# Optimization experiments

Measured on AMD Instinct MI355X. Metric: run time of the kernel, lower is better.

The kernel has to match this reference:

```python
import jax, jax.numpy as jnp
import numpy as np

N, D_IN, D_H, K, E = 100000, 128, 256, 16, 3200000


def setup_inputs() -> dict:
    key = jax.random.key(0)
    ks = jax.random.split(key, 6)
    x = jax.random.normal(ks[0], (N, D_IN), dtype=jnp.float32)
    edge_index = jax.random.randint(ks[1], (2, E), 0, N, dtype=jnp.int64)
    # Linear params (stored as [in, out] for x @ W + b)
    W1 = jax.random.normal(ks[2], (D_IN, D_H), dtype=jnp.float32) * 0.05
    b1 = jnp.zeros((D_H,), dtype=jnp.float32)
    W2 = jax.random.normal(ks[3], (D_H, K), dtype=jnp.float32) * 0.05
    b2 = jnp.zeros((K,), dtype=jnp.float32)
    return {"x": x, "edge_index": edge_index, "W1": W1, "b1": b1, "W2": W2, "b2": b2}


def reference(x, edge_index, W1, b1, W2, b2):
    # 2-layer MLP + row softmax -> soft cluster assignments C [N, K]
    h = jax.nn.relu(x @ W1 + b1)
    C = jax.nn.softmax(h @ W2 + b2, axis=1)
    # trace((C C^T)^T @ adj) == sum over edges (u,v) of C[u] . C[v]
    # (exact, incl. duplicate edges, since to_dense_adj scatter-adds 1 per edge)
    src, dst = edge_index[0], edge_index[1]
    edge_sum = jnp.sum(C[src] * C[dst])  # [E, K] gathered dot products, reduced
    num_edges = jnp.asarray(edge_index.shape[1], dtype=C.dtype)  # adj.sum()
    modularity_loss = -edge_sum / num_edges
    return (C, modularity_loss)
```

## Files before the change

### kernel.cpp

```cpp
#include <hip/hip_runtime.h>

#define N_NODES 100000
#define D_INF   128
#define D_HID   256
#define K_CL    16
#define N_EDGES 3200000
#define N_TILES (N_NODES / 16)

typedef __attribute__((ext_vector_type(8))) __bf16  bf16x8;
typedef __attribute__((ext_vector_type(8))) unsigned short u16x8;
typedef __attribute__((ext_vector_type(4))) float   f32x4;

__device__ __forceinline__ unsigned short f2bf(float f) {
    unsigned int u = __builtin_bit_cast(unsigned int, f);
    u += 0x7fffu + ((u >> 16) & 1u);
    return (unsigned short)(u >> 16);
}
__device__ __forceinline__ float bflo(unsigned int p) {
    return __builtin_bit_cast(float, p << 16);
}
__device__ __forceinline__ float bfhi(unsigned int p) {
    return __builtin_bit_cast(float, p & 0xffff0000u);
}

__global__ void prep_kernel(const float* __restrict__ W1,
                            const float* __restrict__ W2,
                            unsigned short* __restrict__ w1t,
                            unsigned short* __restrict__ w2t,
                            float* __restrict__ acc)
{
    const int i = blockIdx.x * 256 + threadIdx.x;
    if (i == 0) *acc = 0.f;
    if (i < D_INF * D_HID) {
        const int n = i >> 7, k = i & 127;
        w1t[i] = f2bf(W1[k * D_HID + n]);
    }
    if (i < D_HID * K_CL) {
        const int t = i >> 8, n = i & 255;
        w2t[i] = f2bf(W2[n * K_CL + t]);
    }
}

#define W1S 136
#define CHS 40

__global__ __launch_bounds__(256, 2) void mlp_kernel(
    const float* __restrict__ x, const unsigned short* __restrict__ W1T,
    const float* __restrict__ b1, const unsigned short* __restrict__ W2T,
    const float* __restrict__ b2, float* __restrict__ C,
    unsigned short* __restrict__ Cb)
{
    __shared__ unsigned short w1s[256 * W1S];
    __shared__ unsigned short chbuf[4][2][16 * CHS];
    __shared__ float b1s[D_HID];

    const int tid  = threadIdx.x;
    const int wv   = tid >> 6;
    const int lane = tid & 63;
    const int c    = lane & 15;
    const int q    = lane >> 4;

    #pragma unroll
    for (int it = 0; it < 16; ++it) {
        const int idx = it * 256 + tid;
        const int row = idx >> 4, ch = idx & 15;
        const uint4 v = ((const uint4*)W1T)[idx];
        *(uint4*)&w1s[row * W1S + ch * 8] = v;
    }
    if (tid < D_HID) b1s[tid] = b1[tid];

    bf16x8 w2f[8];
    #pragma unroll
    for (int kc2 = 0; kc2 < 8; ++kc2)
        w2f[kc2] = *(const bf16x8*)(W2T + (size_t)c * D_HID + kc2 * 32 + q * 8);
    const float b2v = b2[c];
    __syncthreads();

    unsigned short* const chA = &chbuf[wv][0][0];
    unsigned short* const chB = &chbuf[wv][1][0];

    const int wid     = blockIdx.x * 4 + wv;
    const int wstride = gridDim.x * 4;

    for (int tile = wid; tile < N_TILES; tile += wstride) {
        const int m0 = tile * 16;

        const float* xrow = x + (size_t)(m0 + c) * D_INF + q * 8;
        bf16x8 afr[4];
        #pragma unroll
        for (int kc = 0; kc < 4; ++kc) {
            const float4 xa = *(const float4*)(xrow + kc * 32);
            const float4 xb = *(const float4*)(xrow + kc * 32 + 4);
            u16x8 af;
            af[0] = f2bf(xa.x); af[1] = f2bf(xa.y); af[2] = f2bf(xa.z); af[3] = f2bf(xa.w);
            af[4] = f2bf(xb.x); af[5] = f2bf(xb.y); af[6] = f2bf(xb.z); af[7] = f2bf(xb.w);
            afr[kc] = __builtin_bit_cast(bf16x8, af);
        }

        f32x4 acc2 = (f32x4){0.f, 0.f, 0.f, 0.f};
        #pragma unroll
        for (int kc2 = 0; kc2 < 8; ++kc2) {
            unsigned short* const cb = (kc2 & 1) ? chB : chA;
            #pragma unroll
            for (int half = 0; half < 2; ++half) {
                const int nt = kc2 * 2 + half;
                f32x4 a1 = (f32x4){0.f, 0.f, 0.f, 0.f};
                #pragma unroll
                for (int kc = 0; kc < 4; ++kc) {
                    const bf16x8 bf =
                        *(const bf16x8*)&w1s[(nt * 16 + c) * W1S + kc * 32 + q * 8];
                    a1 = __builtin_amdgcn_mfma_f32_16x16x32_bf16(afr[kc], bf, a1, 0, 0, 0);
                }
                const float bv = b1s[nt * 16 + c];
                #pragma unroll
                for (int r = 0; r < 4; ++r)
                    cb[(4 * q + r) * CHS + half * 16 + c] =
                        f2bf(fmaxf(a1[r] + bv, 0.f));
            }
            const bf16x8 a2 = *(const bf16x8*)&cb[c * CHS + q * 8];
            acc2 = __builtin_amdgcn_mfma_f32_16x16x32_bf16(a2, w2f[kc2], acc2, 0, 0, 0);
        }

        #pragma unroll
        for (int r = 0; r < 4; ++r) {
            const float l = acc2[r] + b2v;
            float mx = l;
            mx = fmaxf(mx, __shfl_xor(mx, 1));
            mx = fmaxf(mx, __shfl_xor(mx, 2));
            mx = fmaxf(mx, __shfl_xor(mx, 4));
            mx = fmaxf(mx, __shfl_xor(mx, 8));
            const float e = __expf(l - mx);
            float sm = e;
            sm += __shfl_xor(sm, 1);
            sm += __shfl_xor(sm, 2);
            sm += __shfl_xor(sm, 4);
            sm += __shfl_xor(sm, 8);
            const float p = e / sm;
            const size_t o = (size_t)(m0 + 4 * q + r) * K_CL + c;
            C[o]  = p;
            Cb[o] = f2bf(p);
        }
    }
}

__global__ __launch_bounds__(256) void edge_kernel(
    const int* __restrict__ ei, const unsigned short* __restrict__ Cb,
    float* __restrict__ acc)
{
    __shared__ float red[4];
    const int tid  = threadIdx.x;
    const int lane = tid & 63;
    const int wv   = tid >> 6;
    const int t    = lane & 3;
    const int g    = lane >> 2;

    const long long wid    = (long long)blockIdx.x * 4 + wv;
    const long long stride = (long long)gridDim.x * 4 * 32;

    float s = 0.f;
    for (long long base = wid * 32; base < N_EDGES; base += stride) {
        const long long e0 = base + g, e1 = e0 + 16;
        const int u0 = ei[e0], v0 = ei[N_EDGES + e0];
        const int u1 = ei[e1], v1 = ei[N_EDGES + e1];
        const uint2 a0 = *(const uint2*)(Cb + (size_t)u0 * K_CL + t * 4);
        const uint2 b0 = *(const uint2*)(Cb + (size_t)v0 * K_CL + t * 4);
        const uint2 a1 = *(const uint2*)(Cb + (size_t)u1 * K_CL + t * 4);
        const uint2 b1 = *(const uint2*)(Cb + (size_t)v1 * K_CL + t * 4);
        s = fmaf(bflo(a0.x), bflo(b0.x), s);
        s = fmaf(bfhi(a0.x), bfhi(b0.x), s);
        s = fmaf(bflo(a0.y), bflo(b0.y), s);
        s = fmaf(bfhi(a0.y), bfhi(b0.y), s);
        s = fmaf(bflo(a1.x), bflo(b1.x), s);
        s = fmaf(bfhi(a1.x), bfhi(b1.x), s);
        s = fmaf(bflo(a1.y), bflo(b1.y), s);
        s = fmaf(bfhi(a1.y), bfhi(b1.y), s);
    }
    s += __shfl_xor(s, 1);
    s += __shfl_xor(s, 2);
    s += __shfl_xor(s, 4);
    s += __shfl_xor(s, 8);
    s += __shfl_xor(s, 16);
    s += __shfl_xor(s, 32);
    if (lane == 0) red[wv] = s;
    __syncthreads();
    if (tid == 0) atomicAdd(acc, red[0] + red[1] + red[2] + red[3]);
}

__global__ void finalize_kernel(const float* __restrict__ acc,
                                float* __restrict__ out)
{
    out[(size_t)N_NODES * K_CL] = -acc[0] / (float)N_EDGES;
}

extern "C" void kernel_launch(void* const* d_in, const int* in_sizes, int n_in,
                              void* d_out, int out_size, void* d_ws, size_t ws_size,
                              hipStream_t stream) {
    const float* x  = (const float*)d_in[0];
    const int*   ei = (const int*)  d_in[1];
    const float* W1 = (const float*)d_in[2];
    const float* b1 = (const float*)d_in[3];
    const float* W2 = (const float*)d_in[4];
    const float* b2 = (const float*)d_in[5];
    float* out = (float*)d_out;

    unsigned short* w1t = (unsigned short*)d_ws;
    unsigned short* w2t = (unsigned short*)((char*)d_ws + 65536);
    float*          acc = (float*)((char*)d_ws + 73728);
    unsigned short* Cb  = (unsigned short*)((char*)d_ws + 73760);

    prep_kernel<<<128, 256, 0, stream>>>(W1, W2, w1t, w2t, acc);
    mlp_kernel<<<512, 256, 0, stream>>>(x, w1t, b1, w2t, b2, out, Cb);
    edge_kernel<<<1024, 256, 0, stream>>>(ei, Cb, acc);
    finalize_kernel<<<1, 1, 0, stream>>>(acc, out);
}
```

Before: 161.1 us.

## Fuse weight prep into MLP, process two tiles per wave, restructure edge gather

Removes the separate prep kernel: each MLP block now converts and transposes W1/W2 from fp32 into shared memory and registers itself, and the accumulator is zeroed with a memset. The MLP loop handles two 16-row tiles per wave so each W1 LDS fragment feeds two MFMAs, and the chunk buffer stride changes. The edge kernel becomes one-shot: each wave loads 128 edge indices coalesced, broadcasts them with shuffles, and gathers a full 16-byte half-row per lane with no grid-stride loop. The cost is redundant per-block weight conversion, scattered 2-byte LDS stores during setup, and more registers.

Result: slower. 240.7 us (+49.4%).

```diff
diff --git a/kernel.cpp b/kernel.cpp
--- a/kernel.cpp
+++ b/kernel.cpp
@@ -5,7 +5,7 @@
 #define D_HID   256
 #define K_CL    16
 #define N_EDGES 3200000
-#define N_TILES (N_NODES / 16)
+#define N_PAIRS 3125
 
 typedef __attribute__((ext_vector_type(8))) __bf16  bf16x8;
 typedef __attribute__((ext_vector_type(8))) unsigned short u16x8;
@@ -23,30 +23,12 @@
     return __builtin_bit_cast(float, p & 0xffff0000u);
 }
 
-__global__ void prep_kernel(const float* __restrict__ W1,
-                            const float* __restrict__ W2,
-                            unsigned short* __restrict__ w1t,
-                            unsigned short* __restrict__ w2t,
-                            float* __restrict__ acc)
-{
-    const int i = blockIdx.x * 256 + threadIdx.x;
-    if (i == 0) *acc = 0.f;
-    if (i < D_INF * D_HID) {
-        const int n = i >> 7, k = i & 127;
-        w1t[i] = f2bf(W1[k * D_HID + n]);
-    }
-    if (i < D_HID * K_CL) {
-        const int t = i >> 8, n = i & 255;
-        w2t[i] = f2bf(W2[n * K_CL + t]);
-    }
-}
-
 #define W1S 136
-#define CHS 40
+#define CHS 36
 
 __global__ __launch_bounds__(256, 2) void mlp_kernel(
-    const float* __restrict__ x, const unsigned short* __restrict__ W1T,
-    const float* __restrict__ b1, const unsigned short* __restrict__ W2T,
+    const float* __restrict__ x,  const float* __restrict__ W1,
+    const float* __restrict__ b1, const float* __restrict__ W2,
     const float* __restrict__ b2, float* __restrict__ C,
     unsigned short* __restrict__ Cb)
 {
@@ -61,84 +43,108 @@
     const int q    = lane >> 4;
 
     #pragma unroll
-    for (int it = 0; it < 16; ++it) {
-        const int idx = it * 256 + tid;
-        const int row = idx >> 4, ch = idx & 15;
-        const uint4 v = ((const uint4*)W1T)[idx];
-        *(uint4*)&w1s[row * W1S + ch * 8] = v;
+    for (int it = 0; it < 32; ++it) {
+        const int idx4 = it * 256 + tid;
+        const int k = idx4 >> 6, n4 = (idx4 & 63) * 4;
+        const float4 v = ((const float4*)W1)[idx4];
+        w1s[(n4 + 0) * W1S + k] = f2bf(v.x);
+        w1s[(n4 + 1) * W1S + k] = f2bf(v.y);
+        w1s[(n4 + 2) * W1S + k] = f2bf(v.z);
+        w1s[(n4 + 3) * W1S + k] = f2bf(v.w);
     }
     if (tid < D_HID) b1s[tid] = b1[tid];
 
     bf16x8 w2f[8];
     #pragma unroll
-    for (int kc2 = 0; kc2 < 8; ++kc2)
-        w2f[kc2] = *(const bf16x8*)(W2T + (size_t)c * D_HID + kc2 * 32 + q * 8);
+    for (int kc2 = 0; kc2 < 8; ++kc2) {
+        u16x8 t;
+        #pragma unroll
+        for (int j = 0; j < 8; ++j)
+            t[j] = f2bf(W2[(kc2 * 32 + q * 8 + j) * K_CL + c]);
+        w2f[kc2] = __builtin_bit_cast(bf16x8, t);
+    }
     const float b2v = b2[c];
     __syncthreads();
 
-    unsigned short* const chA = &chbuf[wv][0][0];
-    unsigned short* const chB = &chbuf[wv][1][0];
+    unsigned short* const cb0 = &chbuf[wv][0][0];
+    unsigned short* const cb1 = &chbuf[wv][1][0];
 
     const int wid     = blockIdx.x * 4 + wv;
     const int wstride = gridDim.x * 4;
 
-    for (int tile = wid; tile < N_TILES; tile += wstride) {
-        const int m0 = tile * 16;
-
-        const float* xrow = x + (size_t)(m0 + c) * D_INF + q * 8;
-        bf16x8 afr[4];
+    for (int pair = wid; pair < N_PAIRS; pair += wstride) {
+        const int m0 = pair * 32;
+
+        const float* xr0 = x + (size_t)(m0 + c) * D_INF + q * 8;
+        const float* xr1 = xr0 + 16 * D_INF;
+        bf16x8 af0[4], af1[4];
         #pragma unroll
         for (int kc = 0; kc < 4; ++kc) {
-            const float4 xa = *(const float4*)(xrow + kc * 32);
-            const float4 xb = *(const float4*)(xrow + kc * 32 + 4);
-            u16x8 af;
-            af[0] = f2bf(xa.x); af[1] = f2bf(xa.y); af[2] = f2bf(xa.z); af[3] = f2bf(xa.w);
-            af[4] = f2bf(xb.x); af[5] = f2bf(xb.y); af[6] = f2bf(xb.z); af[7] = f2bf(xb.w);
-            afr[kc] = __builtin_bit_cast(bf16x8, af);
+            float4 a = *(const float4*)(xr0 + kc * 32);
+            float4 b = *(const float4*)(xr0 + kc * 32 + 4);
+            u16x8 t;
+            t[0] = f2bf(a.x); t[1] = f2bf(a.y); t[2] = f2bf(a.z); t[3] = f2bf(a.w);
+            t[4] = f2bf(b.x); t[5] = f2bf(b.y); t[6] = f2bf(b.z); t[7] = f2bf(b.w);
+            af0[kc] = __builtin_bit_cast(bf16x8, t);
+            a = *(const float4*)(xr1 + kc * 32);
+            b = *(const float4*)(xr1 + kc * 32 + 4);
+            t[0] = f2bf(a.x); t[1] = f2bf(a.y); t[2] = f2bf(a.z); t[3] = f2bf(a.w);
+            t[4] = f2bf(b.x); t[5] = f2bf(b.y); t[6] = f2bf(b.z); t[7] = f2bf(b.w);
+            af1[kc] = __builtin_bit_cast(bf16x8, t);
         }
 
-        f32x4 acc2 = (f32x4){0.f, 0.f, 0.f, 0.f};
+        f32x4 acc2_0 = (f32x4){0.f, 0.f, 0.f, 0.f};
+        f32x4 acc2_1 = (f32x4){0.f, 0.f, 0.f, 0.f};
         #pragma unroll
         for (int kc2 = 0; kc2 < 8; ++kc2) {
-            unsigned short* const cb = (kc2 & 1) ? chB : chA;
             #pragma unroll
             for (int half = 0; half < 2; ++half) {
                 const int nt = kc2 * 2 + half;
-                f32x4 a1 = (f32x4){0.f, 0.f, 0.f, 0.f};
+                f32x4 p0 = (f32x4){0.f, 0.f, 0.f, 0.f};
+                f32x4 p1 = (f32x4){0.f, 0.f, 0.f, 0.f};
                 #pragma unroll
                 for (int kc = 0; kc < 4; ++kc) {
                     const bf16x8 bf =
                         *(const bf16x8*)&w1s[(nt * 16 + c) * W1S + kc * 32 + q * 8];
-                    a1 = __builtin_amdgcn_mfma_f32_16x16x32_bf16(afr[kc], bf, a1, 0, 0, 0);
+                    p0 = __builtin_amdgcn_mfma_f32_16x16x32_bf16(af0[kc], bf, p0, 0, 0, 0);
+                    p1 = __builtin_amdgcn_mfma_f32_16x16x32_bf16(af1[kc], bf, p1, 0, 0, 0);
                 }
                 const float bv = b1s[nt * 16 + c];
                 #pragma unroll
-                for (int r = 0; r < 4; ++r)
-                    cb[(4 * q + r) * CHS + half * 16 + c] =
-                        f2bf(fmaxf(a1[r] + bv, 0.f));
+                for (int r = 0; r < 4; ++r) {
+                    cb0[(4 * q + r) * CHS + half * 16 + c] = f2bf(fmaxf(p0[r] + bv, 0.f));
+                    cb1[(4 * q + r) * CHS + half * 16 + c] = f2bf(fmaxf(p1[r] + bv, 0.f));
+                }
             }
-            const bf16x8 a2 = *(const bf16x8*)&cb[c * CHS + q * 8];
-            acc2 = __builtin_amdgcn_mfma_f32_16x16x32_bf16(a2, w2f[kc2], acc2, 0, 0, 0);
+            const bf16x8 a20 = *(const bf16x8*)&cb0[c * CHS + q * 8];
+            const bf16x8 a21 = *(const bf16x8*)&cb1[c * CHS + q * 8];
+            acc2_0 = __builtin_amdgcn_mfma_f32_16x16x32_bf16(a20, w2f[kc2], acc2_0, 0, 0, 0);
+            acc2_1 = __builtin_amdgcn_mfma_f32_16x16x32_bf16(a21, w2f[kc2], acc2_1, 0, 0, 0);
         }
 
         #pragma unroll
-        for (int r = 0; r < 4; ++r) {
-            const float l = acc2[r] + b2v;
-            float mx = l;
-            mx = fmaxf(mx, __shfl_xor(mx, 1));
-            mx = fmaxf(mx, __shfl_xor(mx, 2));
-            mx = fmaxf(mx, __shfl_xor(mx, 4));
-            mx = fmaxf(mx, __shfl_xor(mx, 8));
-            const float e = __expf(l - mx);
-            float sm = e;
-            sm += __shfl_xor(sm, 1);
-            sm += __shfl_xor(sm, 2);
-            sm += __shfl_xor(sm, 4);
-            sm += __shfl_xor(sm, 8);
-            const float p = e / sm;
-            const size_t o = (size_t)(m0 + 4 * q + r) * K_CL + c;
-            C[o]  = p;
-            Cb[o] = f2bf(p);
+        for (int t2 = 0; t2 < 2; ++t2) {
+            const f32x4 a2 = t2 ? acc2_1 : acc2_0;
+            const int mb = m0 + t2 * 16;
+            #pragma unroll
+            for (int r = 0; r < 4; ++r) {
+                const float l = a2[r] + b2v;
+                float mx = l;
+                mx = fmaxf(mx, __shfl_xor(mx, 1));
+                mx = fmaxf(mx, __shfl_xor(mx, 2));
+                mx = fmaxf(mx, __shfl_xor(mx, 4));
+                mx = fmaxf(mx, __shfl_xor(mx, 8));
+                const float e = __expf(l - mx);
+                float sm = e;
+                sm += __shfl_xor(sm, 1);
+                sm += __shfl_xor(sm, 2);
+                sm += __shfl_xor(sm, 4);
+                sm += __shfl_xor(sm, 8);
+                const float p = e / sm;
+                const size_t o = (size_t)(mb + 4 * q + r) * K_CL + c;
+                C[o]  = p;
+                Cb[o] = f2bf(p);
+            }
         }
     }
 }
@@ -151,29 +157,32 @@
     const int tid  = threadIdx.x;
     const int lane = tid & 63;
     const int wv   = tid >> 6;
-    const int t    = lane & 3;
-    const int g    = lane >> 2;
-
-    const long long wid    = (long long)blockIdx.x * 4 + wv;
-    const long long stride = (long long)gridDim.x * 4 * 32;
+    const int base = (blockIdx.x * 4 + wv) * 128;
+
+    const int u0 = ei[base + lane];
+    const int u1 = ei[base + 64 + lane];
+    const int v0 = ei[N_EDGES + base + lane];
+    const int v1 = ei[N_EDGES + base + 64 + lane];
+
+    const int half8 = (lane & 1) * 8;
+    const int sl    = lane >> 1;
 
     float s = 0.f;
-    for (long long base = wid * 32; base < N_EDGES; base += stride) {
-        const long long e0 = base + g, e1 = e0 + 16;
-        const int u0 = ei[e0], v0 = ei[N_EDGES + e0];
-        const int u1 = ei[e1], v1 = ei[N_EDGES + e1];
-        const uint2 a0 = *(const uint2*)(Cb + (size_t)u0 * K_CL + t * 4);
-        const uint2 b0 = *(const uint2*)(Cb + (size_t)v0 * K_CL + t * 4);
-        const uint2 a1 = *(const uint2*)(Cb + (size_t)u1 * K_CL + t * 4);
-        const uint2 b1 = *(const uint2*)(Cb + (size_t)v1 * K_CL + t * 4);
-        s = fmaf(bflo(a0.x), bflo(b0.x), s);
-        s = fmaf(bfhi(a0.x), bfhi(b0.x), s);
-        s = fmaf(bflo(a0.y), bflo(b0.y), s);
-        s = fmaf(bfhi(a0.y), bfhi(b0.y), s);
-        s = fmaf(bflo(a1.x), bflo(b1.x), s);
-        s = fmaf(bfhi(a1.x), bfhi(b1.x), s);
-        s = fmaf(bflo(a1.y), bflo(b1.y), s);
-        s = fmaf(bfhi(a1.y), bfhi(b1.y), s);
+    #pragma unroll
+    for (int g = 0; g < 4; ++g) {
+        const int src = (g & 1) * 32 + sl;
+        const int ue  = __shfl((g < 2) ? u0 : u1, src);
+        const int ve  = __shfl((g < 2) ? v0 : v1, src);
+        const uint4 a = *(const uint4*)(Cb + (size_t)ue * K_CL + half8);
+        const uint4 b = *(const uint4*)(Cb + (size_t)ve * K_CL + half8);
+        s = fmaf(bflo(a.x), bflo(b.x), s);
+        s = fmaf(bfhi(a.x), bfhi(b.x), s);
+        s = fmaf(bflo(a.y), bflo(b.y), s);
+        s = fmaf(bfhi(a.y), bfhi(b.y), s);
+        s = fmaf(bflo(a.z), bflo(b.z), s);
+        s = fmaf(bfhi(a.z), bfhi(b.z), s);
+        s = fmaf(bflo(a.w), bflo(b.w), s);
+        s = fmaf(bfhi(a.w), bfhi(b.w), s);
     }
     s += __shfl_xor(s, 1);
     s += __shfl_xor(s, 2);
@@ -203,13 +212,11 @@
     const float* b2 = (const float*)d_in[5];
     float* out = (float*)d_out;
 
-    unsigned short* w1t = (unsigned short*)d_ws;
-    unsigned short* w2t = (unsigned short*)((char*)d_ws + 65536);
-    float*          acc = (float*)((char*)d_ws + 73728);
-    unsigned short* Cb  = (unsigned short*)((char*)d_ws + 73760);
-
-    prep_kernel<<<128, 256, 0, stream>>>(W1, W2, w1t, w2t, acc);
-    mlp_kernel<<<512, 256, 0, stream>>>(x, w1t, b1, w2t, b2, out, Cb);
-    edge_kernel<<<1024, 256, 0, stream>>>(ei, Cb, acc);
+    float*          acc = (float*)d_ws;
+    unsigned short* Cb  = (unsigned short*)((char*)d_ws + 64);
+
+    hipMemsetAsync(d_ws, 0, sizeof(float), stream);
+    mlp_kernel<<<512, 256, 0, stream>>>(x, W1, b1, W2, b2, out, Cb);
+    edge_kernel<<<N_EDGES / 512, 256, 0, stream>>>(ei, Cb, acc);
     finalize_kernel<<<1, 1, 0, stream>>>(acc, out);
 }
```
